# Performance work log

Hardware: AMD Instinct MI355X
Metric: run time of the kernel (lower is better)

The kernel has to match this reference:

```python
import jax, jax.numpy as jnp
import numpy as np

B = 32            # decode batch (N flat tokens, q_len=1 each)
D_MODEL = 4096
H = 32            # query heads
HKV = 8           # kv heads (GQA)
HD = 128          # head dim
KVLEN = 2048      # context length per sequence
BLOCK = 256       # paged-cache block size
NBPS = KVLEN // BLOCK          # blocks per sequence = 8
NBLOCKS = B * NBPS             # 256
NSLOTS = NBLOCKS * BLOCK       # 65536
EPS = 1e-6
THETA = 10000.0
NEG = -1e30


def setup_inputs() -> dict:
    key = jax.random.key(0)
    ks = jax.random.split(key, 8)
    seqs = jax.random.normal(ks[0], (B, D_MODEL), dtype=jnp.float32)
    Wq = jax.random.normal(ks[1], (D_MODEL, H * HD), dtype=jnp.float32) * 0.02
    Wk = jax.random.normal(ks[2], (D_MODEL, HKV * HD), dtype=jnp.float32) * 0.02
    Wv = jax.random.normal(ks[3], (D_MODEL, HKV * HD), dtype=jnp.float32) * 0.02
    Wo = jax.random.normal(ks[4], (H * HD, D_MODEL), dtype=jnp.float32) * 0.02
    qn_w = jnp.ones((HD,), dtype=jnp.float32)
    kn_w = jnp.ones((HD,), dtype=jnp.float32)
    k_cache = jax.random.normal(ks[5], (NSLOTS, HKV, HD), dtype=jnp.float32) * 0.02
    v_cache = jax.random.normal(ks[6], (NSLOTS, HKV, HD), dtype=jnp.float32) * 0.02
    # decode step: each seq owns NBPS contiguous blocks; new token goes to last slot
    input_pos = jnp.full((B,), KVLEN - 1, dtype=jnp.int32)
    slot_mapping = (jnp.arange(B, dtype=jnp.int32) * NBPS * BLOCK + (KVLEN - 1)).astype(jnp.int32)
    block_tables = jnp.arange(NBLOCKS, dtype=jnp.int32).reshape(B, NBPS)
    context_lens = jnp.full((B,), KVLEN, dtype=jnp.int32)
    return {
        'seqs': seqs, 'Wq': Wq, 'Wk': Wk, 'Wv': Wv, 'Wo': Wo,
        'qn_w': qn_w, 'kn_w': kn_w, 'k_cache': k_cache, 'v_cache': v_cache,
        'input_pos': input_pos, 'slot_mapping': slot_mapping,
        'block_tables': block_tables, 'context_lens': context_lens,
    }


def _rmsnorm(x, w):
    return x * jax.lax.rsqrt(jnp.mean(x * x, axis=-1, keepdims=True) + EPS) * w


def _rope(x, pos):
    # x: [N, heads, HD], pos: [N]
    half = HD // 2
    inv = 1.0 / (THETA ** (jnp.arange(half, dtype=jnp.float32) / half))
    ang = pos.astype(jnp.float32)[:, None] * inv          # [N, half]
    cos = jnp.cos(ang)[:, None, :]
    sin = jnp.sin(ang)[:, None, :]
    x1, x2 = x[..., :half], x[..., half:]
    return jnp.concatenate([x1 * cos - x2 * sin, x2 * cos + x1 * sin], axis=-1)


def reference(seqs, Wq, Wk, Wv, Wo, qn_w, kn_w, k_cache, v_cache,
              input_pos, slot_mapping, block_tables, context_lens):
    # QKV projections (flat token layout, N = B decode tokens)
    q = (seqs @ Wq).reshape(B, H, HD)
    k = (seqs @ Wk).reshape(B, HKV, HD)
    v = (seqs @ Wv).reshape(B, HKV, HD)
    # qk-norm then RoPE
    q = _rmsnorm(q, qn_w)
    k = _rmsnorm(k, kn_w)
    q = _rope(q, input_pos)
    k = _rope(k, input_pos)
    # paged KV-cache store (slot_mapping scatter)
    kc = k_cache.at[slot_mapping].set(k)
    vc = v_cache.at[slot_mapping].set(v)
    # block-table-indexed gather: slots per sequence [B, KVLEN]
    slots = (block_tables[:, :, None] * BLOCK
             + jnp.arange(BLOCK, dtype=jnp.int32)[None, None, :]).reshape(B, -1)
    K = kc[slots]   # [B, L, HKV, HD]
    V = vc[slots]   # [B, L, HKV, HD]
    L = slots.shape[1]
    # GQA attention: group query heads over kv heads
    G = H // HKV
    qg = q.reshape(B, HKV, G, HD)
    scale = 1.0 / jnp.sqrt(jnp.float32(HD))
    scores = jnp.einsum('bkgd,blkd->bkgl', qg, K) * scale   # [B, HKV, G, L]
    valid = jnp.arange(L, dtype=jnp.int32)[None, :] < context_lens[:, None]
    scores = jnp.where(valid[:, None, None, :], scores, NEG)
    p = jax.nn.softmax(scores, axis=-1)
    out = jnp.einsum('bkgl,blkd->bkgd', p, V).reshape(B, H * HD)
    return out @ Wo
```

## Files before the change

kernel.cpp:

```cpp
#include <hip/hip_runtime.h>
#include <hip/hip_bf16.h>
#include <math.h>

#define B_     32
#define DM_    4096
#define H_     32
#define HKV_   8
#define G_     4
#define HD_    128
#define KVLEN_ 2048
#define NBPS_  8
#define NQKV_  6144
#define KSPLIT_ 16
#define KC_    256
#define ASPLIT_ 16
#define APOS_  128

typedef float vf4 __attribute__((ext_vector_type(4)));
typedef float vf2 __attribute__((ext_vector_type(2)));

__global__ __launch_bounds__(256) void transpose32(
    const float* __restrict__ in, float* __restrict__ out) {
  __shared__ float t[32][65];
  const int tid = threadIdx.x;
  const int k0 = blockIdx.x * 64;
  #pragma unroll
  for (int it = 0; it < 8; ++it) {
    int m = it * 4 + (tid >> 6);
    int k = tid & 63;
    t[m][k] = in[(size_t)m * DM_ + k0 + k];
  }
  __syncthreads();
  #pragma unroll
  for (int it = 0; it < 8; ++it) {
    int flat = it * 256 + tid;
    out[(size_t)k0 * 32 + flat] = t[flat & 31][flat >> 5];
  }
}

__global__ __launch_bounds__(256) void qkv_gemm(
    const float* __restrict__ seqsT, const float* __restrict__ Wq,
    const float* __restrict__ Wk, const float* __restrict__ Wv,
    float* __restrict__ P1) {
  const int tid = threadIdx.x;
  const int nid = blockIdx.x % 24;
  const int kid = blockIdx.x / 24;
  const int k0 = kid * KC_;

  const int ct = tid & 127;
  const int mh16 = __builtin_amdgcn_readfirstlane((tid >> 7) << 4);
  const int n  = nid * 256 + ct * 2;

  const float* W; int col, ldw;
  if (nid < 16)      { W = Wq; col = n;        ldw = 4096; }
  else if (nid < 20) { W = Wk; col = n - 4096; ldw = 1024; }
  else               { W = Wv; col = n - 5120; ldw = 1024; }

  float2 acc[16];
  #pragma unroll
  for (int r = 0; r < 16; ++r) acc[r] = make_float2(0.f, 0.f);

  const vf2* wp = (const vf2*)(W + (size_t)k0 * ldw + col);
  const int ldw2 = ldw >> 1;
  const vf4* ap = (const vf4*)(seqsT + (size_t)k0 * 32 + mh16);

  #pragma unroll 8
  for (int kk = 0; kk < KC_; ++kk) {
    vf2 w = __builtin_nontemporal_load(wp + (size_t)kk * ldw2);
    vf4 a0 = ap[kk * 8 + 0];
    vf4 a1 = ap[kk * 8 + 1];
    vf4 a2 = ap[kk * 8 + 2];
    vf4 a3 = ap[kk * 8 + 3];
    #define FMA2(av, r) \
      acc[r].x = fmaf(av, w.x, acc[r].x); acc[r].y = fmaf(av, w.y, acc[r].y);
    FMA2(a0.x, 0)  FMA2(a0.y, 1)  FMA2(a0.z, 2)  FMA2(a0.w, 3)
    FMA2(a1.x, 4)  FMA2(a1.y, 5)  FMA2(a1.z, 6)  FMA2(a1.w, 7)
    FMA2(a2.x, 8)  FMA2(a2.y, 9)  FMA2(a2.z, 10) FMA2(a2.w, 11)
    FMA2(a3.x, 12) FMA2(a3.y, 13) FMA2(a3.z, 14) FMA2(a3.w, 15)
    #undef FMA2
  }

  float* o = P1 + (size_t)kid * 32 * NQKV_ + n;
  #pragma unroll
  for (int r = 0; r < 16; ++r) {
    int m = mh16 + r;
    *(float2*)(o + (size_t)m * NQKV_) = acc[r];
  }
}

__global__ __launch_bounds__(128) void reduce_norm_rope(
    const float* __restrict__ P1, const float* __restrict__ qn_w,
    const float* __restrict__ kn_w, const int* __restrict__ input_pos,
    float* __restrict__ qf, float* __restrict__ knew, float* __restrict__ vnew) {
  const int b = blockIdx.x / 48;
  const int hh = blockIdx.x % 48;
  const int tid = threadIdx.x;

  int col0, kind;
  if (hh < 32)      { kind = 0; col0 = hh * 128; }
  else if (hh < 40) { kind = 1; col0 = 4096 + (hh - 32) * 128; }
  else              { kind = 2; col0 = 5120 + (hh - 40) * 128; }

  float x = 0.f;
  const float* p = P1 + (size_t)b * NQKV_ + col0 + tid;
  #pragma unroll
  for (int s = 0; s < KSPLIT_; ++s) x += p[(size_t)s * 32 * NQKV_];

  if (kind == 2) {
    vnew[(size_t)b * 1024 + (hh - 40) * 128 + tid] = x;
    return;
  }

  __shared__ float lds[128];
  __shared__ float wred[2];
  float ss = x * x;
  #pragma unroll
  for (int off = 32; off > 0; off >>= 1) ss += __shfl_down(ss, off);
  if ((tid & 63) == 0) wred[tid >> 6] = ss;
  __syncthreads();
  float tot = wred[0] + wred[1];
  float r = rsqrtf(tot * (1.f / 128.f) + 1e-6f);
  const float* wv = (kind == 0) ? qn_w : kn_w;
  x = x * r * wv[tid];

  lds[tid] = x;
  __syncthreads();

  if (tid < 64) {
    float pos = (float)input_pos[b];
    float inv = powf(10000.f, -(float)tid * (1.f / 64.f));
    float ang = pos * inv;
    float c = cosf(ang), s = sinf(ang);
    float x1 = lds[tid], x2 = lds[tid + 64];
    float o1 = x1 * c - x2 * s;
    float o2 = x2 * c + x1 * s;
    float* dst = (kind == 0) ? (qf + (size_t)b * 4096 + hh * 128)
                             : (knew + (size_t)b * 1024 + (hh - 32) * 128);
    dst[tid] = o1;
    dst[tid + 64] = o2;
  }
}

__global__ __launch_bounds__(512) void attn_decode(
    const float* __restrict__ qf, const float* __restrict__ knew,
    const float* __restrict__ vnew, const float* __restrict__ kc,
    const float* __restrict__ vc, const int* __restrict__ block_tables,
    const int* __restrict__ slot_mapping, const int* __restrict__ context_lens,
    float* __restrict__ pacc, float* __restrict__ pls) {
  const int b   = blockIdx.x >> 4;
  const int sp  = blockIdx.x & 15;
  const int tid = threadIdx.x;
  const int w   = tid >> 6;
  const int lane = tid & 63;
  const int gi  = lane >> 4;
  const int l16 = lane & 15;
  const int d0  = l16 * 8;

  const int ctx   = context_lens[b];
  const int fslot = slot_mapping[b];
  const int base  = sp * APOS_;

  const int page  = block_tables[b * NBPS_ + (base >> 8)];
  const int slot0 = (page << 8) + (base & 255);
  const int rel   = fslot - slot0;
  const bool hasf = (rel >= 0) && (rel < APOS_);
  const int nv    = min(APOS_, ctx - base);

  const float scale = 0.08838834764831845f;
  float q[4][8];
  #pragma unroll
  for (int g = 0; g < 4; ++g) {
    const float4* qp = (const float4*)(qf + ((size_t)b * H_ + w * G_ + g) * HD_ + d0);
    float4 a = qp[0], c = qp[1];
    q[g][0] = a.x * scale; q[g][1] = a.y * scale; q[g][2] = a.z * scale; q[g][3] = a.w * scale;
    q[g][4] = c.x * scale; q[g][5] = c.y * scale; q[g][6] = c.z * scale; q[g][7] = c.w * scale;
  }

  const float* knp = knew + ((size_t)b * HKV_ + w) * HD_ + d0;
  const float* vnp = vnew + ((size_t)b * HKV_ + w) * HD_ + d0;
  const float* kcb = kc + ((size_t)slot0 * HKV_ + w) * HD_ + d0;
  const float* vcb = vc + ((size_t)slot0 * HKV_ + w) * HD_ + d0;

  float ls[4] = {0.f, 0.f, 0.f, 0.f};
  float acc[4][8];
  #pragma unroll
  for (int g = 0; g < 4; ++g)
    #pragma unroll
    for (int j = 0; j < 8; ++j) acc[g][j] = 0.f;

  #define ATTN_STEP(K1, K2, V1, V2)                                       \
    {                                                                     \
      float kk8[8] = {K1.x, K1.y, K1.z, K1.w, K2.x, K2.y, K2.z, K2.w};    \
      float vv[8]  = {V1.x, V1.y, V1.z, V1.w, V2.x, V2.y, V2.z, V2.w};    \
      float s[4];                                                         \
      _Pragma("unroll")                                                   \
      for (int g = 0; g < 4; ++g) {                                       \
        float t = 0.f;                                                    \
        _Pragma("unroll")                                                 \
        for (int j = 0; j < 8; ++j) t = fmaf(q[g][j], kk8[j], t);         \
        s[g] = t;                                                         \
      }                                                                   \
      _Pragma("unroll")                                                   \
      for (int o2 = 1; o2 < 16; o2 <<= 1) {                               \
        _Pragma("unroll")                                                 \
        for (int g = 0; g < 4; ++g) s[g] += __shfl_xor(s[g], o2);         \
      }                                                                   \
      _Pragma("unroll")                                                   \
      for (int g = 0; g < 4; ++g) {                                       \
        float pw = __expf(s[g]);                                          \
        ls[g] += pw;                                                      \
        _Pragma("unroll")                                                 \
        for (int j = 0; j < 8; ++j) acc[g][j] = fmaf(pw, vv[j], acc[g][j]); \
      }                                                                   \
    }

  if (!hasf && nv == APOS_) {
    #pragma unroll 2
    for (int it = 0; it < APOS_ / 4; ++it) {
      const int off = it * 4 + gi;
      const vf4* kp4 = (const vf4*)(kcb + (size_t)off * (HKV_ * HD_));
      const vf4* vp4 = (const vf4*)(vcb + (size_t)off * (HKV_ * HD_));
      vf4 k1 = __builtin_nontemporal_load(kp4);
      vf4 k2 = __builtin_nontemporal_load(kp4 + 1);
      vf4 v1 = __builtin_nontemporal_load(vp4);
      vf4 v2 = __builtin_nontemporal_load(vp4 + 1);
      ATTN_STEP(k1, k2, v1, v2)
    }
  } else {
    for (int it = 0; it < APOS_ / 4; ++it) {
      const int off = it * 4 + gi;
      if (base + off < ctx) {
        const float* kp = (off == rel) ? knp : (kcb + (size_t)off * (HKV_ * HD_));
        const float* vp = (off == rel) ? vnp : (vcb + (size_t)off * (HKV_ * HD_));
        float4 k1 = ((const float4*)kp)[0];
        float4 k2 = ((const float4*)kp)[1];
        float4 v1 = ((const float4*)vp)[0];
        float4 v2 = ((const float4*)vp)[1];
        ATTN_STEP(k1, k2, v1, v2)
      }
    }
  }
  #undef ATTN_STEP

  #pragma unroll
  for (int o2 = 16; o2 < 64; o2 <<= 1) {
    #pragma unroll
    for (int g = 0; g < 4; ++g) {
      ls[g] += __shfl_xor(ls[g], o2);
      #pragma unroll
      for (int j = 0; j < 8; ++j) acc[g][j] += __shfl_xor(acc[g][j], o2);
    }
  }

  if (gi == 0) {
    #pragma unroll
    for (int g = 0; g < 4; ++g) {
      float* dst = pacc + (((size_t)sp * B_ + b) * H_ + (w * G_ + g)) * HD_ + d0;
      float4 o1 = {acc[g][0], acc[g][1], acc[g][2], acc[g][3]};
      float4 o2 = {acc[g][4], acc[g][5], acc[g][6], acc[g][7]};
      ((float4*)dst)[0] = o1;
      ((float4*)dst)[1] = o2;
      if (l16 == 0) pls[((size_t)sp * B_ + b) * H_ + (w * G_ + g)] = ls[g];
    }
  }
}

__global__ __launch_bounds__(256) void attn_merge(
    const float* __restrict__ pacc, const float* __restrict__ pls,
    float* __restrict__ attnb) {
  const int idx = blockIdx.x * 256 + threadIdx.x;
  const int bh  = idx >> 5;
  const float4* p4 = (const float4*)pacc;
  float4 A = {0.f, 0.f, 0.f, 0.f};
  float L = 0.f;
  #pragma unroll
  for (int sp = 0; sp < ASPLIT_; ++sp) {
    float4 t = p4[(size_t)sp * 32768 + idx];
    A.x += t.x; A.y += t.y; A.z += t.z; A.w += t.w;
    L += pls[sp * (B_ * H_) + bh];
  }
  float r = 1.f / L;
  A.x *= r; A.y *= r; A.z *= r; A.w *= r;
  ((float4*)attnb)[idx] = A;
}

__global__ __launch_bounds__(512) void oproj_gemm(
    const float* __restrict__ attnT, const float* __restrict__ Wo,
    float* __restrict__ P2) {
  const int tid = threadIdx.x;
  const int nid = blockIdx.x & 15;
  const int kid = blockIdx.x >> 4;
  const int k0 = kid * KC_;

  const int ct = tid & 127;
  const int mq8 = __builtin_amdgcn_readfirstlane((tid >> 7) << 3);
  const int n  = nid * 256 + ct * 2;

  float2 acc[8];
  #pragma unroll
  for (int r = 0; r < 8; ++r) acc[r] = make_float2(0.f, 0.f);

  const vf2* wp = (const vf2*)(Wo + (size_t)k0 * 4096 + n);
  const vf4* ap = (const vf4*)(attnT + (size_t)k0 * 32 + mq8);

  #pragma unroll 8
  for (int kk = 0; kk < KC_; ++kk) {
    vf2 w = __builtin_nontemporal_load(wp + (size_t)kk * 2048);
    vf4 a0 = ap[kk * 8 + 0];
    vf4 a1 = ap[kk * 8 + 1];
    #define FMA2(av, r) \
      acc[r].x = fmaf(av, w.x, acc[r].x); acc[r].y = fmaf(av, w.y, acc[r].y);
    FMA2(a0.x, 0) FMA2(a0.y, 1) FMA2(a0.z, 2) FMA2(a0.w, 3)
    FMA2(a1.x, 4) FMA2(a1.y, 5) FMA2(a1.z, 6) FMA2(a1.w, 7)
    #undef FMA2
  }

  float* o = P2 + (size_t)kid * 32 * 4096 + n;
  #pragma unroll
  for (int r = 0; r < 8; ++r) {
    int m = mq8 + r;
    *(float2*)(o + (size_t)m * 4096) = acc[r];
  }
}

__global__ __launch_bounds__(256) void oproj_reduce(
    const float* __restrict__ P2, float* __restrict__ out) {
  const int idx = blockIdx.x * 256 + threadIdx.x;
  float s = 0.f;
  #pragma unroll
  for (int t = 0; t < KSPLIT_; ++t) s += P2[(size_t)t * 131072 + idx];
  out[idx] = s;
}

extern "C" void kernel_launch(void* const* d_in, const int* in_sizes, int n_in,
                              void* d_out, int out_size, void* d_ws, size_t ws_size,
                              hipStream_t stream) {
  const float* seqs = (const float*)d_in[0];
  const float* Wq   = (const float*)d_in[1];
  const float* Wk   = (const float*)d_in[2];
  const float* Wv   = (const float*)d_in[3];
  const float* Wo   = (const float*)d_in[4];
  const float* qn_w = (const float*)d_in[5];
  const float* kn_w = (const float*)d_in[6];
  const float* kc   = (const float*)d_in[7];
  const float* vc   = (const float*)d_in[8];
  const int* input_pos = (const int*)d_in[9];
  const int* slot_map  = (const int*)d_in[10];
  const int* btab      = (const int*)d_in[11];
  const int* ctx       = (const int*)d_in[12];
  float* out = (float*)d_out;

  char* w = (char*)d_ws;
  float* seqsT = (float*)(w);
  float* P1    = (float*)(w + 1048576);
  float* qf    = (float*)(w + 14680064);
  float* knew  = (float*)(w + 15204352);
  float* vnew  = (float*)(w + 15335424);
  float* attnb = (float*)(w + 15466496);
  float* attnT = (float*)(w + 15990784);
  float* pacc  = (float*)(w + 16515072);
  float* pls   = (float*)(w + 24903680);
  float* P2    = (float*)(w + 24969216);

  transpose32<<<64, 256, 0, stream>>>(seqs, seqsT);
  qkv_gemm<<<24 * KSPLIT_, 256, 0, stream>>>(seqsT, Wq, Wk, Wv, P1);
  reduce_norm_rope<<<B_ * 48, 128, 0, stream>>>(P1, qn_w, kn_w, input_pos, qf, knew, vnew);
  attn_decode<<<B_ * ASPLIT_, 512, 0, stream>>>(qf, knew, vnew, kc, vc, btab, slot_map, ctx, pacc, pls);
  attn_merge<<<128, 256, 0, stream>>>(pacc, pls, attnb);
  transpose32<<<64, 256, 0, stream>>>(attnb, attnT);
  oproj_gemm<<<16 * KSPLIT_, 512, 0, stream>>>(attnT, Wo, P2);
  oproj_reduce<<<512, 256, 0, stream>>>(P2, out);
}
```

Baseline: 205.0 us.

## Restage GEMM activations in LDS, widen weight loads, fuse merge-transpose, fix attention fast path

Both GEMMs now stage the transposed activation tile in shared memory and have each thread load float4 weight columns, with the K-split doubled (KSPLIT 32, KC 128). The oproj reduce is vectorized to float4. The attention merge writes its output already transposed, which removes one transpose launch. The attention kernel keeps the fast nontemporal path even when the new token falls in the chunk: it subtracts the stale cache entry's contribution and adds the new one, at the cost of some cancellation error. Doubling KSPLIT also doubles the partial-sum traffic that the reduce kernels must read.

```diff
diff --git a/kernel.cpp b/kernel.cpp
--- a/kernel.cpp
+++ b/kernel.cpp
@@ -11,13 +11,12 @@
 #define KVLEN_ 2048
 #define NBPS_  8
 #define NQKV_  6144
-#define KSPLIT_ 16
-#define KC_    256
+#define KSPLIT_ 32
+#define KC_    128
 #define ASPLIT_ 16
 #define APOS_  128
 
 typedef float vf4 __attribute__((ext_vector_type(4)));
-typedef float vf2 __attribute__((ext_vector_type(2)));
 
 __global__ __launch_bounds__(256) void transpose32(
     const float* __restrict__ in, float* __restrict__ out) {
@@ -47,44 +46,53 @@
   const int kid = blockIdx.x / 24;
   const int k0 = kid * KC_;
 
-  const int ct = tid & 127;
-  const int mh16 = __builtin_amdgcn_readfirstlane((tid >> 7) << 4);
-  const int n  = nid * 256 + ct * 2;
+  __shared__ __align__(16) float sT[KC_][36];
+  const float4* src = (const float4*)(seqsT + (size_t)k0 * 32);
+  #pragma unroll
+  for (int it = 0; it < 4; ++it) {
+    int flat = it * 256 + tid;
+    int kk = flat >> 3, m4 = (flat & 7) * 4;
+    *(float4*)&sT[kk][m4] = src[flat];
+  }
+  __syncthreads();
+
+  const int ct = tid & 63;
+  const int wv = tid >> 6;
+  const int n  = nid * 256 + ct * 4;
 
   const float* W; int col, ldw;
   if (nid < 16)      { W = Wq; col = n;        ldw = 4096; }
   else if (nid < 20) { W = Wk; col = n - 4096; ldw = 1024; }
   else               { W = Wv; col = n - 5120; ldw = 1024; }
 
-  float2 acc[16];
-  #pragma unroll
-  for (int r = 0; r < 16; ++r) acc[r] = make_float2(0.f, 0.f);
-
-  const vf2* wp = (const vf2*)(W + (size_t)k0 * ldw + col);
-  const int ldw2 = ldw >> 1;
-  const vf4* ap = (const vf4*)(seqsT + (size_t)k0 * 32 + mh16);
+  float4 acc[8];
+  #pragma unroll
+  for (int r = 0; r < 8; ++r) acc[r] = make_float4(0.f, 0.f, 0.f, 0.f);
+
+  const vf4* wp = (const vf4*)(W + (size_t)k0 * ldw + col);
+  const int ldw4 = ldw >> 2;
+  const float4* arow = (const float4*)&sT[0][wv * 8];
 
   #pragma unroll 8
   for (int kk = 0; kk < KC_; ++kk) {
-    vf2 w = __builtin_nontemporal_load(wp + (size_t)kk * ldw2);
-    vf4 a0 = ap[kk * 8 + 0];
-    vf4 a1 = ap[kk * 8 + 1];
-    vf4 a2 = ap[kk * 8 + 2];
-    vf4 a3 = ap[kk * 8 + 3];
-    #define FMA2(av, r) \
-      acc[r].x = fmaf(av, w.x, acc[r].x); acc[r].y = fmaf(av, w.y, acc[r].y);
-    FMA2(a0.x, 0)  FMA2(a0.y, 1)  FMA2(a0.z, 2)  FMA2(a0.w, 3)
-    FMA2(a1.x, 4)  FMA2(a1.y, 5)  FMA2(a1.z, 6)  FMA2(a1.w, 7)
-    FMA2(a2.x, 8)  FMA2(a2.y, 9)  FMA2(a2.z, 10) FMA2(a2.w, 11)
-    FMA2(a3.x, 12) FMA2(a3.y, 13) FMA2(a3.z, 14) FMA2(a3.w, 15)
-    #undef FMA2
+    vf4 w = __builtin_nontemporal_load(wp + (size_t)kk * ldw4);
+    float4 a0 = arow[kk * 9];
+    float4 a1 = arow[kk * 9 + 1];
+    #define FMA4(av, r)                          \
+      acc[r].x = fmaf(av, w.x, acc[r].x);        \
+      acc[r].y = fmaf(av, w.y, acc[r].y);        \
+      acc[r].z = fmaf(av, w.z, acc[r].z);        \
+      acc[r].w = fmaf(av, w.w, acc[r].w);
+    FMA4(a0.x, 0) FMA4(a0.y, 1) FMA4(a0.z, 2) FMA4(a0.w, 3)
+    FMA4(a1.x, 4) FMA4(a1.y, 5) FMA4(a1.z, 6) FMA4(a1.w, 7)
+    #undef FMA4
   }
 
   float* o = P1 + (size_t)kid * 32 * NQKV_ + n;
   #pragma unroll
-  for (int r = 0; r < 16; ++r) {
-    int m = mh16 + r;
-    *(float2*)(o + (size_t)m * NQKV_) = acc[r];
+  for (int r = 0; r < 8; ++r) {
+    int m = wv * 8 + r;
+    *(float4*)(o + (size_t)m * NQKV_) = acc[r];
   }
 }
 
@@ -188,7 +196,7 @@
     #pragma unroll
     for (int j = 0; j < 8; ++j) acc[g][j] = 0.f;
 
-  #define ATTN_STEP(K1, K2, V1, V2)                                       \
+  #define ATTN_STEP(K1, K2, V1, V2, SGN)                                  \
     {                                                                     \
       float kk8[8] = {K1.x, K1.y, K1.z, K1.w, K2.x, K2.y, K2.z, K2.w};    \
       float vv[8]  = {V1.x, V1.y, V1.z, V1.w, V2.x, V2.y, V2.z, V2.w};    \
@@ -207,14 +215,14 @@
       }                                                                   \
       _Pragma("unroll")                                                   \
       for (int g = 0; g < 4; ++g) {                                       \
-        float pw = __expf(s[g]);                                          \
+        float pw = (SGN) * __expf(s[g]);                                  \
         ls[g] += pw;                                                      \
         _Pragma("unroll")                                                 \
         for (int j = 0; j < 8; ++j) acc[g][j] = fmaf(pw, vv[j], acc[g][j]); \
       }                                                                   \
     }
 
-  if (!hasf && nv == APOS_) {
+  if (nv == APOS_) {
     #pragma unroll 2
     for (int it = 0; it < APOS_ / 4; ++it) {
       const int off = it * 4 + gi;
@@ -224,7 +232,21 @@
       vf4 k2 = __builtin_nontemporal_load(kp4 + 1);
       vf4 v1 = __builtin_nontemporal_load(vp4);
       vf4 v2 = __builtin_nontemporal_load(vp4 + 1);
-      ATTN_STEP(k1, k2, v1, v2)
+      ATTN_STEP(k1, k2, v1, v2, 1.f)
+    }
+    if (hasf && gi == (rel & 3)) {
+      const float* kps = kcb + (size_t)rel * (HKV_ * HD_);
+      const float* vps = vcb + (size_t)rel * (HKV_ * HD_);
+      float4 k1 = ((const float4*)kps)[0];
+      float4 k2 = ((const float4*)kps)[1];
+      float4 v1 = ((const float4*)vps)[0];
+      float4 v2 = ((const float4*)vps)[1];
+      ATTN_STEP(k1, k2, v1, v2, -1.f)
+      float4 f1 = ((const float4*)knp)[0];
+      float4 f2 = ((const float4*)knp)[1];
+      float4 g1 = ((const float4*)vnp)[0];
+      float4 g2 = ((const float4*)vnp)[1];
+      ATTN_STEP(f1, f2, g1, g2, 1.f)
     }
   } else {
     for (int it = 0; it < APOS_ / 4; ++it) {
@@ -236,7 +258,7 @@
         float4 k2 = ((const float4*)kp)[1];
         float4 v1 = ((const float4*)vp)[0];
         float4 v2 = ((const float4*)vp)[1];
-        ATTN_STEP(k1, k2, v1, v2)
+        ATTN_STEP(k1, k2, v1, v2, 1.f)
       }
     }
   }
@@ -265,10 +287,13 @@
   }
 }
 
-__global__ __launch_bounds__(256) void attn_merge(
+__global__ __launch_bounds__(256) void attn_mergeT(
     const float* __restrict__ pacc, const float* __restrict__ pls,
-    float* __restrict__ attnb) {
+    float* __restrict__ attnT) {
   const int idx = blockIdx.x * 256 + threadIdx.x;
+  const int b   = idx >> 10;
+  const int h   = (idx >> 5) & 31;
+  const int d4  = (idx & 31) * 4;
   const int bh  = idx >> 5;
   const float4* p4 = (const float4*)pacc;
   float4 A = {0.f, 0.f, 0.f, 0.f};
@@ -280,11 +305,14 @@
     L += pls[sp * (B_ * H_) + bh];
   }
   float r = 1.f / L;
-  A.x *= r; A.y *= r; A.z *= r; A.w *= r;
-  ((float4*)attnb)[idx] = A;
-}
-
-__global__ __launch_bounds__(512) void oproj_gemm(
+  float* dst = attnT + ((size_t)(h * 128 + d4)) * 32 + b;
+  dst[0]  = A.x * r;
+  dst[32] = A.y * r;
+  dst[64] = A.z * r;
+  dst[96] = A.w * r;
+}
+
+__global__ __launch_bounds__(256) void oproj_gemm(
     const float* __restrict__ attnT, const float* __restrict__ Wo,
     float* __restrict__ P2) {
   const int tid = threadIdx.x;
@@ -292,44 +320,61 @@
   const int kid = blockIdx.x >> 4;
   const int k0 = kid * KC_;
 
-  const int ct = tid & 127;
-  const int mq8 = __builtin_amdgcn_readfirstlane((tid >> 7) << 3);
-  const int n  = nid * 256 + ct * 2;
-
-  float2 acc[8];
-  #pragma unroll
-  for (int r = 0; r < 8; ++r) acc[r] = make_float2(0.f, 0.f);
-
-  const vf2* wp = (const vf2*)(Wo + (size_t)k0 * 4096 + n);
-  const vf4* ap = (const vf4*)(attnT + (size_t)k0 * 32 + mq8);
+  __shared__ __align__(16) float sT[KC_][36];
+  const float4* src = (const float4*)(attnT + (size_t)k0 * 32);
+  #pragma unroll
+  for (int it = 0; it < 4; ++it) {
+    int flat = it * 256 + tid;
+    int kk = flat >> 3, m4 = (flat & 7) * 4;
+    *(float4*)&sT[kk][m4] = src[flat];
+  }
+  __syncthreads();
+
+  const int ct = tid & 63;
+  const int wv = tid >> 6;
+  const int n  = nid * 256 + ct * 4;
+
+  float4 acc[8];
+  #pragma unroll
+  for (int r = 0; r < 8; ++r) acc[r] = make_float4(0.f, 0.f, 0.f, 0.f);
+
+  const vf4* wp = (const vf4*)(Wo + (size_t)k0 * 4096 + n);
+  const float4* arow = (const float4*)&sT[0][wv * 8];
 
   #pragma unroll 8
   for (int kk = 0; kk < KC_; ++kk) {
-    vf2 w = __builtin_nontemporal_load(wp + (size_t)kk * 2048);
-    vf4 a0 = ap[kk * 8 + 0];
-    vf4 a1 = ap[kk * 8 + 1];
-    #define FMA2(av, r) \
-      acc[r].x = fmaf(av, w.x, acc[r].x); acc[r].y = fmaf(av, w.y, acc[r].y);
-    FMA2(a0.x, 0) FMA2(a0.y, 1) FMA2(a0.z, 2) FMA2(a0.w, 3)
-    FMA2(a1.x, 4) FMA2(a1.y, 5) FMA2(a1.z, 6) FMA2(a1.w, 7)
-    #undef FMA2
+    vf4 w = __builtin_nontemporal_load(wp + (size_t)kk * 1024);
+    float4 a0 = arow[kk * 9];
+    float4 a1 = arow[kk * 9 + 1];
+    #define FMA4(av, r)                          \
+      acc[r].x = fmaf(av, w.x, acc[r].x);        \
+      acc[r].y = fmaf(av, w.y, acc[r].y);        \
+      acc[r].z = fmaf(av, w.z, acc[r].z);        \
+      acc[r].w = fmaf(av, w.w, acc[r].w);
+    FMA4(a0.x, 0) FMA4(a0.y, 1) FMA4(a0.z, 2) FMA4(a0.w, 3)
+    FMA4(a1.x, 4) FMA4(a1.y, 5) FMA4(a1.z, 6) FMA4(a1.w, 7)
+    #undef FMA4
   }
 
   float* o = P2 + (size_t)kid * 32 * 4096 + n;
   #pragma unroll
   for (int r = 0; r < 8; ++r) {
-    int m = mq8 + r;
-    *(float2*)(o + (size_t)m * 4096) = acc[r];
+    int m = wv * 8 + r;
+    *(float4*)(o + (size_t)m * 4096) = acc[r];
   }
 }
 
 __global__ __launch_bounds__(256) void oproj_reduce(
     const float* __restrict__ P2, float* __restrict__ out) {
   const int idx = blockIdx.x * 256 + threadIdx.x;
-  float s = 0.f;
-  #pragma unroll
-  for (int t = 0; t < KSPLIT_; ++t) s += P2[(size_t)t * 131072 + idx];
-  out[idx] = s;
+  const float4* p4 = (const float4*)P2;
+  float4 s = {0.f, 0.f, 0.f, 0.f};
+  #pragma unroll
+  for (int t = 0; t < KSPLIT_; ++t) {
+    float4 v = p4[(size_t)t * 32768 + idx];
+    s.x += v.x; s.y += v.y; s.z += v.z; s.w += v.w;
+  }
+  ((float4*)out)[idx] = s;
 }
 
 extern "C" void kernel_launch(void* const* d_in, const int* in_sizes, int n_in,
@@ -352,22 +397,20 @@
 
   char* w = (char*)d_ws;
   float* seqsT = (float*)(w);
-  float* P1    = (float*)(w + 1048576);
-  float* qf    = (float*)(w + 14680064);
-  float* knew  = (float*)(w + 15204352);
-  float* vnew  = (float*)(w + 15335424);
-  float* attnb = (float*)(w + 15466496);
-  float* attnT = (float*)(w + 15990784);
-  float* pacc  = (float*)(w + 16515072);
-  float* pls   = (float*)(w + 24903680);
-  float* P2    = (float*)(w + 24969216);
+  float* P1    = (float*)(w + 524288);
+  float* qf    = (float*)(w + 25690112);
+  float* knew  = (float*)(w + 26214400);
+  float* vnew  = (float*)(w + 26345472);
+  float* attnT = (float*)(w + 26476544);
+  float* pacc  = (float*)(w + 27000832);
+  float* pls   = (float*)(w + 35389440);
+  float* P2    = (float*)(w + 35454976);
 
   transpose32<<<64, 256, 0, stream>>>(seqs, seqsT);
   qkv_gemm<<<24 * KSPLIT_, 256, 0, stream>>>(seqsT, Wq, Wk, Wv, P1);
   reduce_norm_rope<<<B_ * 48, 128, 0, stream>>>(P1, qn_w, kn_w, input_pos, qf, knew, vnew);
   attn_decode<<<B_ * ASPLIT_, 512, 0, stream>>>(qf, knew, vnew, kc, vc, btab, slot_map, ctx, pacc, pls);
-  attn_merge<<<128, 256, 0, stream>>>(pacc, pls, attnb);
-  transpose32<<<64, 256, 0, stream>>>(attnb, attnT);
-  oproj_gemm<<<16 * KSPLIT_, 512, 0, stream>>>(attnT, Wo, P2);
-  oproj_reduce<<<512, 256, 0, stream>>>(P2, out);
-}
+  attn_mergeT<<<128, 256, 0, stream>>>(pacc, pls, attnT);
+  oproj_gemm<<<16 * KSPLIT_, 256, 0, stream>>>(attnT, Wo, P2);
+  oproj_reduce<<<128, 256, 0, stream>>>(P2, out);
+}
```

Result: slower. 219.5 us (+7.1%).

## Retune QKV split-K, fuse merge with transpose, fast-path fresh-token attention, vectorize reduce

Applied to the files above, without the earlier changes.

The QKV GEMM split-K factor goes from 16 to 32 chunks of 128, giving more blocks for parallelism at the cost of a larger partial buffer and a longer reduction. The attention merge now writes the transposed layout directly, which removes a separate transpose launch. Blocks that contain the freshly written token now take the vectorized fast loop and then correct for it by subtracting the stale cache contribution and adding the new K/V, instead of using the slow branchy loop. The unroll factor on that loop goes from 2 to 4, and the output reduction now uses float4 loads.

```diff
diff --git a/kernel.cpp b/kernel.cpp
--- a/kernel.cpp
+++ b/kernel.cpp
@@ -11,8 +11,10 @@
 #define KVLEN_ 2048
 #define NBPS_  8
 #define NQKV_  6144
-#define KSPLIT_ 16
-#define KC_    256
+#define QKSPLIT_ 32
+#define QKC_     128
+#define OKSPLIT_ 16
+#define OKC_     256
 #define ASPLIT_ 16
 #define APOS_  128
 
@@ -45,7 +47,7 @@
   const int tid = threadIdx.x;
   const int nid = blockIdx.x % 24;
   const int kid = blockIdx.x / 24;
-  const int k0 = kid * KC_;
+  const int k0 = kid * QKC_;
 
   const int ct = tid & 127;
   const int mh16 = __builtin_amdgcn_readfirstlane((tid >> 7) << 4);
@@ -65,7 +67,7 @@
   const vf4* ap = (const vf4*)(seqsT + (size_t)k0 * 32 + mh16);
 
   #pragma unroll 8
-  for (int kk = 0; kk < KC_; ++kk) {
+  for (int kk = 0; kk < QKC_; ++kk) {
     vf2 w = __builtin_nontemporal_load(wp + (size_t)kk * ldw2);
     vf4 a0 = ap[kk * 8 + 0];
     vf4 a1 = ap[kk * 8 + 1];
@@ -104,7 +106,7 @@
   float x = 0.f;
   const float* p = P1 + (size_t)b * NQKV_ + col0 + tid;
   #pragma unroll
-  for (int s = 0; s < KSPLIT_; ++s) x += p[(size_t)s * 32 * NQKV_];
+  for (int s = 0; s < QKSPLIT_; ++s) x += p[(size_t)s * 32 * NQKV_];
 
   if (kind == 2) {
     vnew[(size_t)b * 1024 + (hh - 40) * 128 + tid] = x;
@@ -188,7 +190,7 @@
     #pragma unroll
     for (int j = 0; j < 8; ++j) acc[g][j] = 0.f;
 
-  #define ATTN_STEP(K1, K2, V1, V2)                                       \
+  #define ATTN_STEP(K1, K2, V1, V2, SGN)                                  \
     {                                                                     \
       float kk8[8] = {K1.x, K1.y, K1.z, K1.w, K2.x, K2.y, K2.z, K2.w};    \
       float vv[8]  = {V1.x, V1.y, V1.z, V1.w, V2.x, V2.y, V2.z, V2.w};    \
@@ -207,15 +209,15 @@
       }                                                                   \
       _Pragma("unroll")                                                   \
       for (int g = 0; g < 4; ++g) {                                       \
-        float pw = __expf(s[g]);                                          \
+        float pw = (SGN) * __expf(s[g]);                                  \
         ls[g] += pw;                                                      \
         _Pragma("unroll")                                                 \
         for (int j = 0; j < 8; ++j) acc[g][j] = fmaf(pw, vv[j], acc[g][j]); \
       }                                                                   \
     }
 
-  if (!hasf && nv == APOS_) {
-    #pragma unroll 2
+  if (nv == APOS_) {
+    #pragma unroll 4
     for (int it = 0; it < APOS_ / 4; ++it) {
       const int off = it * 4 + gi;
       const vf4* kp4 = (const vf4*)(kcb + (size_t)off * (HKV_ * HD_));
@@ -224,7 +226,21 @@
       vf4 k2 = __builtin_nontemporal_load(kp4 + 1);
       vf4 v1 = __builtin_nontemporal_load(vp4);
       vf4 v2 = __builtin_nontemporal_load(vp4 + 1);
-      ATTN_STEP(k1, k2, v1, v2)
+      ATTN_STEP(k1, k2, v1, v2, 1.f)
+    }
+    if (hasf && gi == (rel & 3)) {
+      const float* kps = kcb + (size_t)rel * (HKV_ * HD_);
+      const float* vps = vcb + (size_t)rel * (HKV_ * HD_);
+      float4 k1 = ((const float4*)kps)[0];
+      float4 k2 = ((const float4*)kps)[1];
+      float4 v1 = ((const float4*)vps)[0];
+      float4 v2 = ((const float4*)vps)[1];
+      ATTN_STEP(k1, k2, v1, v2, -1.f)
+      float4 f1 = ((const float4*)knp)[0];
+      float4 f2 = ((const float4*)knp)[1];
+      float4 g1 = ((const float4*)vnp)[0];
+      float4 g2 = ((const float4*)vnp)[1];
+      ATTN_STEP(f1, f2, g1, g2, 1.f)
     }
   } else {
     for (int it = 0; it < APOS_ / 4; ++it) {
@@ -236,7 +252,7 @@
         float4 k2 = ((const float4*)kp)[1];
         float4 v1 = ((const float4*)vp)[0];
         float4 v2 = ((const float4*)vp)[1];
-        ATTN_STEP(k1, k2, v1, v2)
+        ATTN_STEP(k1, k2, v1, v2, 1.f)
       }
     }
   }
@@ -265,10 +281,13 @@
   }
 }
 
-__global__ __launch_bounds__(256) void attn_merge(
+__global__ __launch_bounds__(256) void attn_mergeT(
     const float* __restrict__ pacc, const float* __restrict__ pls,
-    float* __restrict__ attnb) {
+    float* __restrict__ attnT) {
   const int idx = blockIdx.x * 256 + threadIdx.x;
+  const int b   = idx >> 10;
+  const int h   = (idx >> 5) & 31;
+  const int d4  = (idx & 31) * 4;
   const int bh  = idx >> 5;
   const float4* p4 = (const float4*)pacc;
   float4 A = {0.f, 0.f, 0.f, 0.f};
@@ -280,8 +299,11 @@
     L += pls[sp * (B_ * H_) + bh];
   }
   float r = 1.f / L;
-  A.x *= r; A.y *= r; A.z *= r; A.w *= r;
-  ((float4*)attnb)[idx] = A;
+  float* dst = attnT + ((size_t)(h * 128 + d4)) * 32 + b;
+  dst[0]  = A.x * r;
+  dst[32] = A.y * r;
+  dst[64] = A.z * r;
+  dst[96] = A.w * r;
 }
 
 __global__ __launch_bounds__(512) void oproj_gemm(
@@ -290,7 +312,7 @@
   const int tid = threadIdx.x;
   const int nid = blockIdx.x & 15;
   const int kid = blockIdx.x >> 4;
-  const int k0 = kid * KC_;
+  const int k0 = kid * OKC_;
 
   const int ct = tid & 127;
   const int mq8 = __builtin_amdgcn_readfirstlane((tid >> 7) << 3);
@@ -304,7 +326,7 @@
   const vf4* ap = (const vf4*)(attnT + (size_t)k0 * 32 + mq8);
 
   #pragma unroll 8
-  for (int kk = 0; kk < KC_; ++kk) {
+  for (int kk = 0; kk < OKC_; ++kk) {
     vf2 w = __builtin_nontemporal_load(wp + (size_t)kk * 2048);
     vf4 a0 = ap[kk * 8 + 0];
     vf4 a1 = ap[kk * 8 + 1];
@@ -326,10 +348,14 @@
 __global__ __launch_bounds__(256) void oproj_reduce(
     const float* __restrict__ P2, float* __restrict__ out) {
   const int idx = blockIdx.x * 256 + threadIdx.x;
-  float s = 0.f;
-  #pragma unroll
-  for (int t = 0; t < KSPLIT_; ++t) s += P2[(size_t)t * 131072 + idx];
-  out[idx] = s;
+  const float4* p4 = (const float4*)P2;
+  float4 s = {0.f, 0.f, 0.f, 0.f};
+  #pragma unroll
+  for (int t = 0; t < OKSPLIT_; ++t) {
+    float4 v = p4[(size_t)t * 32768 + idx];
+    s.x += v.x; s.y += v.y; s.z += v.z; s.w += v.w;
+  }
+  ((float4*)out)[idx] = s;
 }
 
 extern "C" void kernel_launch(void* const* d_in, const int* in_sizes, int n_in,
@@ -352,22 +378,20 @@
 
   char* w = (char*)d_ws;
   float* seqsT = (float*)(w);
-  float* P1    = (float*)(w + 1048576);
-  float* qf    = (float*)(w + 14680064);
-  float* knew  = (float*)(w + 15204352);
-  float* vnew  = (float*)(w + 15335424);
-  float* attnb = (float*)(w + 15466496);
-  float* attnT = (float*)(w + 15990784);
-  float* pacc  = (float*)(w + 16515072);
-  float* pls   = (float*)(w + 24903680);
-  float* P2    = (float*)(w + 24969216);
+  float* P1    = (float*)(w + 524288);
+  float* qf    = (float*)(w + 25690112);
+  float* knew  = (float*)(w + 26214400);
+  float* vnew  = (float*)(w + 26345472);
+  float* attnT = (float*)(w + 26476544);
+  float* pacc  = (float*)(w + 27000832);
+  float* pls   = (float*)(w + 35389440);
+  float* P2    = (float*)(w + 35454976);
 
   transpose32<<<64, 256, 0, stream>>>(seqs, seqsT);
-  qkv_gemm<<<24 * KSPLIT_, 256, 0, stream>>>(seqsT, Wq, Wk, Wv, P1);
+  qkv_gemm<<<24 * QKSPLIT_, 256, 0, stream>>>(seqsT, Wq, Wk, Wv, P1);
   reduce_norm_rope<<<B_ * 48, 128, 0, stream>>>(P1, qn_w, kn_w, input_pos, qf, knew, vnew);
   attn_decode<<<B_ * ASPLIT_, 512, 0, stream>>>(qf, knew, vnew, kc, vc, btab, slot_map, ctx, pacc, pls);
-  attn_merge<<<128, 256, 0, stream>>>(pacc, pls, attnb);
-  transpose32<<<64, 256, 0, stream>>>(attnb, attnT);
-  oproj_gemm<<<16 * KSPLIT_, 512, 0, stream>>>(attnT, Wo, P2);
-  oproj_reduce<<<512, 256, 0, stream>>>(P2, out);
-}
+  attn_mergeT<<<128, 256, 0, stream>>>(pacc, pls, attnT);
+  oproj_gemm<<<16 * OKSPLIT_, 512, 0, stream>>>(attnT, Wo, P2);
+  oproj_reduce<<<128, 256, 0, stream>>>(P2, out);
+}
```

New measurement: 195.3 us. 1.05x faster.
